# Performance work log

Measured on AMD Instinct MI355X. Metric: run time of the kernel, lower is better.

## Reference

```python
import jax, jax.numpy as jnp
import numpy as np

N, E, D, V, MAX_EDGES, G, ITERS = 50000, 200000, 128, 2000, 3, 256, 2


def _mlp3(h, W1, b1, W2, b2, W3, b3):
    h = jax.nn.relu(h @ W1 + b1)
    h = jax.nn.relu(h @ W2 + b2)
    return jax.nn.relu(h @ W3 + b3)


def _enc(ids, emb, W1, b1, W2, b2):
    h = emb[ids]
    h = jax.nn.relu(h @ W1 + b1)
    return jax.nn.relu(h @ W2 + b2)


def setup_inputs():
    key = jax.random.key(0)
    ks = iter(jax.random.split(key, 64))

    def p(shape):
        return jax.random.normal(next(ks), shape, jnp.float32) * 0.02

    inp = {
        'x': jax.random.randint(next(ks), (N,), 0, V),
        'edge_index': jax.random.randint(next(ks), (2, E), 0, N),
        'edge_attr': jax.random.randint(next(ks), (E,), 0, MAX_EDGES),
        'batch_vec': jnp.sort(jax.random.randint(next(ks), (N,), 0, G)),
        'emb_node': p((V, 2 * D)), 'Wn1': p((2 * D, D)), 'bn1': jnp.zeros((D,), jnp.float32),
        'Wn2': p((D, D)), 'bn2': jnp.zeros((D,), jnp.float32),
        'emb_edge': p((MAX_EDGES, 2 * D)), 'We1': p((2 * D, D)), 'be1': jnp.zeros((D,), jnp.float32),
        'We2': p((D, D)), 'be2': jnp.zeros((D,), jnp.float32),
    }
    for tag in ('p', 'c', 'f'):  # parent_agg, child_agg, final_agg 3-layer MLPs
        inp['W' + tag + '1'] = p((3 * D, 2 * D)); inp['b' + tag + '1'] = jnp.zeros((2 * D,), jnp.float32)
        inp['W' + tag + '2'] = p((2 * D, D)); inp['b' + tag + '2'] = jnp.zeros((D,), jnp.float32)
        inp['W' + tag + '3'] = p((D, D)); inp['b' + tag + '3'] = jnp.zeros((D,), jnp.float32)
    inp['Wo1'] = p((D, 4 * D)); inp['bo1'] = jnp.zeros((4 * D,), jnp.float32)
    inp['Wo2'] = p((4 * D, 8 * D)); inp['bo2'] = jnp.zeros((8 * D,), jnp.float32)
    return inp


def reference(x, edge_index, edge_attr, batch_vec, emb_node, Wn1, bn1, Wn2, bn2,
              emb_edge, We1, be1, We2, be2,
              Wp1, bp1, Wp2, bp2, Wp3, bp3,
              Wc1, bc1, Wc2, bc2, Wc3, bc3,
              Wf1, bf1, Wf2, bf2, Wf3, bf3,
              Wo1, bo1, Wo2, bo2):
    nodes = _enc(x, emb_node, Wn1, bn1, Wn2, bn2)       # [N, D]
    ea = _enc(edge_attr, emb_edge, We1, be1, We2, be2)  # [E, D]
    src, dst = edge_index[0], edge_index[1]
    # both aggregations normalize by degree of edge_index[0] (as in the source)
    deg = jax.ops.segment_sum(jnp.ones((E,), nodes.dtype), src, num_segments=N)
    deg_inv = jnp.where(deg > 0, 1.0 / deg, 0.0)[:, None]  # [N, 1]
    for _ in range(ITERS):
        # parent agg: flow source_to_target -> x_i = nodes[dst], x_j = nodes[src], sum at dst
        mp = _mlp3(jnp.concatenate([nodes[dst], nodes[src], ea], axis=1), Wp1, bp1, Wp2, bp2, Wp3, bp3)
        fi = deg_inv * jax.ops.segment_sum(mp, dst, num_segments=N)
        # child agg: flow target_to_source -> x_i = nodes[src], x_j = nodes[dst], sum at src
        mc = _mlp3(jnp.concatenate([nodes[src], nodes[dst], ea], axis=1), Wc1, bc1, Wc2, bc2, Wc3, bc3)
        fo = deg_inv * jax.ops.segment_sum(mc, src, num_segments=N)
        upd = _mlp3(jnp.concatenate([nodes, fi, fo], axis=1), Wf1, bf1, Wf2, bf2, Wf3, bf3)
        nodes = nodes + upd
    h = jax.nn.relu(nodes @ Wo1 + bo1)
    h = jax.nn.relu(h @ Wo2 + bo2)                      # [N, 8D]
    return jax.ops.segment_max(h, batch_vec, num_segments=G)  # global max pool [G, 8D]
```

## Files before the change

### kernel.cpp

```cpp
#include <hip/hip_runtime.h>

#define NN 50000
#define NE 200000
#define DD 128
#define GG 256
#define NITERS 2
#define NBINS 50176
#define NPART 196

typedef unsigned short u16;
typedef unsigned int u32;
typedef __bf16 bf16x8 __attribute__((ext_vector_type(8)));
typedef float f32x4 __attribute__((ext_vector_type(4)));

union U16x8 { uint4 u; bf16x8 v; u16 s[8]; };

__device__ __forceinline__ u16 f2b(float f) {
    u32 u = __float_as_uint(f);
    return (u16)((u + 0x7FFFu + ((u >> 16) & 1u)) >> 16);
}
__device__ __forceinline__ float b2f(u16 s) { return __uint_as_float(((u32)s) << 16); }

__device__ __forceinline__ uint2 pack4(const float* v) {
    uint2 r;
    r.x = (u32)f2b(v[0]) | ((u32)f2b(v[1]) << 16);
    r.y = (u32)f2b(v[2]) | ((u32)f2b(v[3]) << 16);
    return r;
}

__device__ __forceinline__ void gload_lds16(const void* g, void* lds) {
    __builtin_amdgcn_global_load_lds((const __attribute__((address_space(1))) void*)g,
                                     (__attribute__((address_space(3))) void*)lds, 16, 0, 0);
}

__device__ __forceinline__ int xcd_swz(int orig, int nwg) {
    int q = nwg >> 3, r = nwg & 7;
    int x = orig & 7, loc = orig >> 3;
    return (x < r ? x * (q + 1) : r * (q + 1) + (x - r) * q) + loc;
}

template<int K, int NL, int EPI, bool RELU, int LDN>
__global__ __launch_bounds__(256) void expand_k(
    const u16* __restrict__ A, const uint4* __restrict__ wfrag,
    const float* __restrict__ bias, float* __restrict__ of, u16* __restrict__ ob,
    int M)
{
    constexpr int KS = K / 32;
    __shared__ uint4 smem[K * 16];
    const int t = threadIdx.x, l = t & 63, wv = t >> 6;
    const int mh = wv >> 1, nh = wv & 1;
    const int mblk = blockIdx.x;
    const int c = blockIdx.y;

    #pragma unroll
    for (int i = 0; i < K / 16; ++i) {
        int s = t + 256 * i;
        int ln = s & 63, mt = (s >> 6) & 7, ksl = s >> 9;
        int row = mblk * 128 + mt * 16 + (ln & 15);
        if (row >= M) row = M - 1;
        int kk = ksl * 32 + (ln >> 4) * 8;
        gload_lds16(A + (size_t)row * K + kk, &smem[s - ln]);
    }
    __syncthreads();

    f32x4 acc[4][4] = {};
    #pragma unroll
    for (int ksl = 0; ksl < KS; ++ksl) {
        uint4 wa[4];
        #pragma unroll
        for (int mi = 0; mi < 4; ++mi)
            wa[mi] = wfrag[(size_t)((c * KS + ksl) * 8 + mh * 4 + mi) * 64 + l];
        bf16x8 bn[4];
        #pragma unroll
        for (int ni = 0; ni < 4; ++ni) { U16x8 u; u.u = smem[(ksl * 8 + nh * 4 + ni) * 64 + l]; bn[ni] = u.v; }
        #pragma unroll
        for (int mi = 0; mi < 4; ++mi) {
            U16x8 u; u.u = wa[mi];
            #pragma unroll
            for (int ni = 0; ni < 4; ++ni)
                acc[mi][ni] = __builtin_amdgcn_mfma_f32_16x16x32_bf16(u.v, bn[ni], acc[mi][ni], 0, 0, 0);
        }
    }
    float4 bb[4];
    #pragma unroll
    for (int mi = 0; mi < 4; ++mi) {
        if (bias) bb[mi] = *(const float4*)(bias + c * 128 + mh * 64 + mi * 16 + 4 * (l >> 4));
        else { bb[mi].x = 0.f; bb[mi].y = 0.f; bb[mi].z = 0.f; bb[mi].w = 0.f; }
    }
    #pragma unroll
    for (int ni = 0; ni < 4; ++ni) {
        int node = mblk * 128 + nh * 64 + ni * 16 + (l & 15);
        if (node >= M) continue;
        #pragma unroll
        for (int mi = 0; mi < 4; ++mi) {
            int col = c * 128 + mh * 64 + mi * 16 + 4 * (l >> 4);
            float v[4];
            const float* bf = &bb[mi].x;
            #pragma unroll
            for (int r = 0; r < 4; ++r) {
                v[r] = acc[mi][ni][r] + bf[r];
                if (RELU) v[r] = fmaxf(v[r], 0.f);
            }
            if (EPI == 0) {
                *(uint2*)(ob + (size_t)node * LDN + col) = pack4(v);
            } else {
                size_t a = (size_t)node * 128 + col;
                if (EPI == 2) {
                    float4 old = *(const float4*)(of + a);
                    v[0] += old.x; v[1] += old.y; v[2] += old.z; v[3] += old.w;
                }
                float4 s4; s4.x = v[0]; s4.y = v[1]; s4.z = v[2]; s4.w = v[3];
                *(float4*)(of + a) = s4;
                *(uint2*)(ob + a) = pack4(v);
            }
        }
    }
}

struct SrcBf16 {
    static constexpr bool DIRECT = true;
    const u16* A; int K;
    __device__ const void* gaddr(int row, int kk) const { return A + (size_t)row * K + kk; }
    __device__ bf16x8 operator()(int row, int kk) const {
        U16x8 u; u.u = *(const uint4*)(A + (size_t)row * K + kk); return u.v;
    }
};
struct SrcEnc {
    static constexpr bool DIRECT = false;
    const float* emb; const int* xids;
    __device__ const void* gaddr(int, int) const { return nullptr; }
    __device__ bf16x8 operator()(int row, int kk) const {
        int n = xids[row];
        const float* p = emb + (size_t)n * 256 + kk;
        float4 f0 = *(const float4*)p, f1 = *(const float4*)(p + 4);
        U16x8 r;
        r.s[0]=f2b(f0.x); r.s[1]=f2b(f0.y); r.s[2]=f2b(f0.z); r.s[3]=f2b(f0.w);
        r.s[4]=f2b(f1.x); r.s[5]=f2b(f1.y); r.s[6]=f2b(f1.z); r.s[7]=f2b(f1.w);
        return r.v;
    }
};
struct SrcUpd {
    static constexpr bool DIRECT = false;
    const float* nodes; const float* fi; const float* fo; const int* deg;
    __device__ const void* gaddr(int, int) const { return nullptr; }
    __device__ bf16x8 operator()(int row, int kk) const {
        const float* s; float sc = 1.f;
        if (kk < 128) s = nodes + (size_t)row * 128 + kk;
        else {
            int d = deg[row];
            sc = d > 0 ? 1.f / (float)d : 0.f;
            s = (kk < 256) ? fi + (size_t)row * 128 + (kk - 128)
                           : fo + (size_t)row * 128 + (kk - 256);
        }
        float4 f0 = *(const float4*)s, f1 = *(const float4*)(s + 4);
        U16x8 r;
        r.s[0]=f2b(f0.x*sc); r.s[1]=f2b(f0.y*sc); r.s[2]=f2b(f0.z*sc); r.s[3]=f2b(f0.w*sc);
        r.s[4]=f2b(f1.x*sc); r.s[5]=f2b(f1.y*sc); r.s[6]=f2b(f1.z*sc); r.s[7]=f2b(f1.w*sc);
        return r.v;
    }
};

struct EpiArgs { float* of; u16* ob; const int* idx; int ldN; };

template<int KDIM, int NBLK, int EPI, bool RELU, class SRC>
__global__ __launch_bounds__(256) void gemm_k(SRC src, const uint4* __restrict__ wfrag,
                                              const float* __restrict__ bias,
                                              EpiArgs ea, int M)
{
    constexpr int KS = KDIM / 32;
    constexpr int NPANEL = KDIM / 64;
    __shared__ uint4 smem[2048];
    const int t = threadIdx.x;
    const int l = t & 63;
    const int wv = t >> 6;
    const int mh = wv >> 1, nh = wv & 1;
    const int ell = xcd_swz(blockIdx.x, gridDim.x);
    const int mblk = ell / NBLK, nblk = ell % NBLK;

    f32x4 acc[4][4] = {};

    for (int p = 0; p < NPANEL; ++p) {
        __syncthreads();
        if constexpr (SRC::DIRECT) {
            #pragma unroll
            for (int i = 0; i < 4; ++i) {
                int s = t + 256 * i;
                int ln = s & 63, mt = (s >> 6) & 7, ksl = s >> 9;
                int row = mblk * 128 + mt * 16 + (ln & 15);
                if (row >= M) row = M - 1;
                int kk = p * 64 + ksl * 32 + (ln >> 4) * 8;
                gload_lds16(src.gaddr(row, kk), &smem[s - ln]);
            }
        } else {
            #pragma unroll
            for (int i = 0; i < 4; ++i) {
                int s = t + 256 * i;
                int ln = s & 63, mt = (s >> 6) & 7, ksl = s >> 9;
                int row = mblk * 128 + mt * 16 + (ln & 15);
                if (row >= M) row = M - 1;
                int kk = p * 64 + ksl * 32 + (ln >> 4) * 8;
                U16x8 u; u.v = src(row, kk);
                smem[s] = u.u;
            }
        }
        {
            const uint4* wp = wfrag + (size_t)(nblk * KS + 2 * p) * 512;
            #pragma unroll
            for (int i = 0; i < 4; ++i) {
                int s = t + 256 * i;
                gload_lds16(wp + s, &smem[1024 + (s - (s & 63))]);
            }
        }
        __syncthreads();
        #pragma unroll
        for (int ksl = 0; ksl < 2; ++ksl) {
            bf16x8 a[4], b[4];
            #pragma unroll
            for (int mi = 0; mi < 4; ++mi) { U16x8 u; u.u = smem[(ksl*8 + mh*4 + mi)*64 + l]; a[mi] = u.v; }
            #pragma unroll
            for (int ni = 0; ni < 4; ++ni) { U16x8 u; u.u = smem[1024 + (ksl*8 + nh*4 + ni)*64 + l]; b[ni] = u.v; }
            #pragma unroll
            for (int mi = 0; mi < 4; ++mi)
                #pragma unroll
                for (int ni = 0; ni < 4; ++ni)
                    acc[mi][ni] = __builtin_amdgcn_mfma_f32_16x16x32_bf16(a[mi], b[ni], acc[mi][ni], 0, 0, 0);
        }
    }

    float bcol[4];
    #pragma unroll
    for (int ni = 0; ni < 4; ++ni)
        bcol[ni] = bias ? bias[nblk * 128 + nh * 64 + ni * 16 + (l & 15)] : 0.f;

    if (EPI == 0) {
        __syncthreads();
        u16* bn = (u16*)smem;
        #pragma unroll
        for (int mi = 0; mi < 4; ++mi)
            #pragma unroll
            for (int ni = 0; ni < 4; ++ni)
                #pragma unroll
                for (int r = 0; r < 4; ++r) {
                    int rl = mh * 64 + mi * 16 + (l >> 4) * 4 + r;
                    int cl = nh * 64 + ni * 16 + (l & 15);
                    float v = acc[mi][ni][r] + bcol[ni];
                    if (RELU) v = fmaxf(v, 0.f);
                    int sx = (rl >> 2) & 7;
                    bn[rl * 128 + ((((cl >> 3) ^ sx)) << 3) + (cl & 7)] = f2b(v);
                }
        __syncthreads();
        int row = t >> 1, half = t & 1;
        int grow = mblk * 128 + row;
        if (grow < M) {
            int sx = (row >> 2) & 7;
            uint4* dst = (uint4*)(ea.ob + (size_t)grow * ea.ldN + nblk * 128 + half * 64);
            const uint4* sp = ((const uint4*)bn) + row * 16;
            #pragma unroll
            for (int i = 0; i < 8; ++i) dst[i] = sp[(half * 8 + i) ^ sx];
        }
    } else if (EPI == 3) {
        int g16[4][4];
        #pragma unroll
        for (int mi = 0; mi < 4; ++mi) {
            int rb = mblk * 128 + mh * 64 + mi * 16 + (l >> 4) * 4;
            #pragma unroll
            for (int r = 0; r < 4; ++r)
                g16[mi][r] = (rb + r < M) ? ea.idx[rb + r] : -1;
        }
        #pragma unroll
        for (int ni = 0; ni < 4; ++ni) {
            int colg = nblk * 128 + nh * 64 + ni * 16 + (l & 15);
            float mv = 0.f; int cg = -1;
            #pragma unroll
            for (int mi = 0; mi < 4; ++mi)
                #pragma unroll
                for (int r = 0; r < 4; ++r) {
                    float v = acc[mi][ni][r] + bcol[ni];
                    if (RELU) v = fmaxf(v, 0.f);
                    int g = g16[mi][r];
                    if (g != cg) {
                        if (cg >= 0) atomicMax((u32*)(ea.of + (size_t)cg * 1024 + colg), __float_as_uint(mv));
                        cg = g; mv = v;
                    } else mv = fmaxf(mv, v);
                }
            if (cg >= 0) atomicMax((u32*)(ea.of + (size_t)cg * 1024 + colg), __float_as_uint(mv));
        }
    }
}

__global__ __launch_bounds__(256) void edge_fused(
    const u16* __restrict__ P, const float* __restrict__ T,
    const uint4* __restrict__ W2f, const float* __restrict__ b2,
    const uint4* __restrict__ W3f, const float* __restrict__ b3,
    const int* __restrict__ idxA, const int* __restrict__ idxB,
    const int* __restrict__ eattr, float* __restrict__ agg)
{
    __shared__ uint4 smA[2048];
    __shared__ int   sidx[3][128];
    __shared__ float sT[768];
    const int t = threadIdx.x;
    const int l = t & 63;
    const int wv = t >> 6;
    const int mh = wv >> 1, nh = wv & 1;
    const int base = xcd_swz(blockIdx.x, gridDim.x) * 128;

    if (t < 128) {
        int e = (base + t < NE) ? base + t : NE - 1;
        sidx[0][t] = idxA[e];
        sidx[1][t] = idxB[e];
        sidx[2][t] = eattr[e];
    }
    for (int i = t; i < 768; i += 256) sT[i] = T[i];
    __syncthreads();

    const int rt0 = wv * 16 + (l & 15);
    const int rt1 = (wv + 4) * 16 + (l & 15);
    const int klo = (l >> 4) * 8;
    const u16* pA[2] = { P + (size_t)sidx[0][rt0] * 512, P + (size_t)sidx[0][rt1] * 512 };
    const u16* pB[2] = { P + (size_t)sidx[1][rt0] * 512 + 256, P + (size_t)sidx[1][rt1] * 512 + 256 };
    const float* pT[2] = { sT + sidx[2][rt0] * 256, sT + sidx[2][rt1] * 256 };

    uint4 ra[4], rb[4];
    #pragma unroll
    for (int i = 0; i < 4; ++i) {
        int kk = (i >> 1) * 32 + klo;
        ra[i] = *(const uint4*)(pA[i & 1] + kk);
        rb[i] = *(const uint4*)(pB[i & 1] + kk);
    }

    f32x4 acc[4][4] = {};
    #pragma unroll
    for (int p = 0; p < 4; ++p) {
        #pragma unroll
        for (int i = 0; i < 4; ++i) {
            int kk = (i >> 1) * 32 + klo;
            U16x8 ua, ub, r;
            ua.u = ra[i]; ub.u = rb[i];
            const float* tb = pT[i & 1] + p * 64 + kk;
            #pragma unroll
            for (int j = 0; j < 8; ++j) {
                float v = b2f(ua.s[j]) + b2f(ub.s[j]) + tb[j];
                r.s[j] = f2b(fmaxf(v, 0.f));
            }
            smA[(p & 1) * 1024 + t + 256 * i] = r.u;
            if (p < 3) {
                int kn = (p + 1) * 64 + kk;
                ra[i] = *(const uint4*)(pA[i & 1] + kn);
                rb[i] = *(const uint4*)(pB[i & 1] + kn);
            }
        }
        asm volatile("s_waitcnt lgkmcnt(0)" ::: "memory");
        __builtin_amdgcn_s_barrier();
        uint4 bw[2][4];
        #pragma unroll
        for (int ksl = 0; ksl < 2; ++ksl)
            #pragma unroll
            for (int ni = 0; ni < 4; ++ni)
                bw[ksl][ni] = W2f[(size_t)((p * 2 + ksl) * 8 + nh * 4 + ni) * 64 + l];
        #pragma unroll
        for (int ksl = 0; ksl < 2; ++ksl) {
            bf16x8 a[4];
            #pragma unroll
            for (int mi = 0; mi < 4; ++mi) { U16x8 u; u.u = smA[(p & 1) * 1024 + (ksl*8 + mh*4 + mi)*64 + l]; a[mi] = u.v; }
            #pragma unroll
            for (int mi = 0; mi < 4; ++mi)
                #pragma unroll
                for (int ni = 0; ni < 4; ++ni) {
                    U16x8 u; u.u = bw[ksl][ni];
                    acc[mi][ni] = __builtin_amdgcn_mfma_f32_16x16x32_bf16(a[mi], u.v, acc[mi][ni], 0, 0, 0);
                }
        }
    }

    float bc2[4];
    #pragma unroll
    for (int ni = 0; ni < 4; ++ni) bc2[ni] = b2[nh * 64 + ni * 16 + (l & 15)];
    __builtin_amdgcn_s_barrier();
    u16* bn = (u16*)smA;
    #pragma unroll
    for (int mi = 0; mi < 4; ++mi)
        #pragma unroll
        for (int ni = 0; ni < 4; ++ni)
            #pragma unroll
            for (int r = 0; r < 4; ++r) {
                int rl = mh * 64 + mi * 16 + (l >> 4) * 4 + r;
                int cl = nh * 64 + ni * 16 + (l & 15);
                float v = fmaxf(acc[mi][ni][r] + bc2[ni], 0.f);
                int sx = (rl >> 2) & 7;
                bn[rl * 128 + (((cl >> 3) ^ sx) << 3) + (cl & 7)] = f2b(v);
            }
    asm volatile("s_waitcnt lgkmcnt(0)" ::: "memory");
    __builtin_amdgcn_s_barrier();

    f32x4 acc2[4][4] = {};
    #pragma unroll
    for (int ks = 0; ks < 4; ++ks) {
        uint4 bw[4];
        #pragma unroll
        for (int ni = 0; ni < 4; ++ni)
            bw[ni] = W3f[(size_t)(ks * 8 + nh * 4 + ni) * 64 + l];
        bf16x8 a[4];
        #pragma unroll
        for (int mi = 0; mi < 4; ++mi) {
            int rl = (mh * 4 + mi) * 16 + (l & 15);
            int c0 = ks * 32 + (l >> 4) * 8;
            int sx = (rl >> 2) & 7;
            U16x8 u; u.u = *(const uint4*)&bn[rl * 128 + (((c0 >> 3) ^ sx) << 3)];
            a[mi] = u.v;
        }
        #pragma unroll
        for (int mi = 0; mi < 4; ++mi)
            #pragma unroll
            for (int ni = 0; ni < 4; ++ni) {
                U16x8 u; u.u = bw[ni];
                acc2[mi][ni] = __builtin_amdgcn_mfma_f32_16x16x32_bf16(a[mi], u.v, acc2[mi][ni], 0, 0, 0);
            }
    }

    float bc3[4];
    #pragma unroll
    for (int ni = 0; ni < 4; ++ni) bc3[ni] = b3[nh * 64 + ni * 16 + (l & 15)];
    #pragma unroll
    for (int mi = 0; mi < 4; ++mi) {
        int rt4 = mh * 64 + mi * 16 + (l >> 4) * 4;
        int nd[4];
        #pragma unroll
        for (int r = 0; r < 4; ++r)
            nd[r] = (base + rt4 + r < NE) ? sidx[0][rt4 + r] : -1;
        #pragma unroll
        for (int ni = 0; ni < 4; ++ni) {
            int col = nh * 64 + ni * 16 + (l & 15);
            float mv = 0.f; int cg = -1;
            #pragma unroll
            for (int r = 0; r < 4; ++r) {
                float v = fmaxf(acc2[mi][ni][r] + bc3[ni], 0.f);
                if (nd[r] != cg) {
                    if (cg >= 0) atomicAdd(agg + (size_t)cg * 128 + col, mv);
                    cg = nd[r]; mv = v;
                } else mv += v;
            }
            if (cg >= 0) atomicAdd(agg + (size_t)cg * 128 + col, mv);
        }
    }
}

__global__ void hist2_kernel(const int* __restrict__ dstI, const int* __restrict__ srcI,
                             int* __restrict__ hist)
{
    int i = blockIdx.x * 256 + threadIdx.x;
    if (i < NE) atomicAdd(&hist[dstI[i]], 1);
    else if (i < 2 * NE) atomicAdd(&hist[NBINS + srcI[i - NE]], 1);
}
__global__ void chunk_sum(const int* __restrict__ h, int* __restrict__ part)
{
    __shared__ int sh[256];
    int t = threadIdx.x, b = blockIdx.x;
    sh[t] = h[b * 256 + t];
    __syncthreads();
    for (int o = 128; o > 0; o >>= 1) { if (t < o) sh[t] += sh[t + o]; __syncthreads(); }
    if (t == 0) part[b] = sh[0];
}
__global__ void scan_part2(int* part)
{
    __shared__ int sh[256];
    int t = threadIdx.x, b = blockIdx.x;
    int* p = part + b * NPART;
    sh[t] = (t < NPART) ? p[t] : 0;
    __syncthreads();
    for (int o = 1; o < 256; o <<= 1) {
        int x = (t >= o) ? sh[t - o] : 0;
        __syncthreads(); sh[t] += x; __syncthreads();
    }
    if (t < NPART) p[t] = (t ? sh[t - 1] : 0) + b * NE;
}
__global__ void mk_cursor(const int* __restrict__ h, const int* __restrict__ part,
                          int* __restrict__ cur)
{
    __shared__ int sh[256];
    int t = threadIdx.x, b = blockIdx.x;
    int v = h[b * 256 + t];
    sh[t] = v;
    __syncthreads();
    for (int o = 1; o < 256; o <<= 1) {
        int x = (t >= o) ? sh[t - o] : 0;
        __syncthreads(); sh[t] += x; __syncthreads();
    }
    cur[b * 256 + t] = part[b] + sh[t] - v;
}
__global__ void sort_scatter2(const int* __restrict__ dstI, const int* __restrict__ srcI,
                              const int* __restrict__ at, int* __restrict__ cur,
                              int* __restrict__ oA, int* __restrict__ oB, int* __restrict__ oC)
{
    int i = blockIdx.x * 256 + threadIdx.x;
    if (i < NE) {
        int k = dstI[i];
        int p = atomicAdd(&cur[k], 1);
        oA[p] = k; oB[p] = srcI[i]; oC[p] = at[i];
    } else if (i < 2 * NE) {
        int e = i - NE;
        int k = srcI[e];
        int p = atomicAdd(&cur[NBINS + k], 1);
        oA[p] = k; oB[p] = dstI[e]; oC[p] = at[e];
    }
}

struct PackPtrs { const float* p[13]; };

__global__ void pack_all(PackPtrs pp, uint4* __restrict__ frag)
{
    int tid = blockIdx.x * 256 + threadIdx.x;
    if (tid >= 126976) return;
    constexpr int NJ = 15;
    const int   start[NJ] = {0,4096,6144,10240,14336,18432,22528,26624,28672,32768,34816,47104,51200,53248,61440};
    const int   fbase[NJ] = {0,4096,6144,6144,14336,14336,22528,26624,28672,32768,34816,47104,51200,53248,61440};
    const short wsel [NJ] = {0,1,2,2,3,3,4,5,6,7,8,9,10,11,12};
    const short ldt  [NJ] = {128,128,256,256,256,256,128,128,128,128,256,128,128,512,1024};
    const short rot  [NJ] = {0,0,0,128,0,128,0,0,0,0,0,0,0,0,0};
    const short cot  [NJ] = {0,0,0,-256,0,-256,0,0,0,0,0,0,0,0,0};
    const short nbst [NJ] = {0,0,0,2,0,2,0,0,0,0,0,0,0,0,0};
    const short kst  [NJ] = {8,4,4,4,4,4,8,4,8,4,12,8,4,4,16};
    int j = 0;
    for (int i = NJ - 1; i >= 1; --i) if (tid >= start[i]) { j = i; break; }
    int rem = tid - start[j];
    int KS = kst[j];
    int nbrel = rem / (KS * 512);
    int r1 = rem % (KS * 512);
    int ks = r1 >> 9;
    int r2 = r1 & 511;
    int nt = r2 >> 6, l = r2 & 63;
    int nb = nbst[j] + nbrel;
    int k  = ks * 32 + (l >> 4) * 8;
    int ld = ldt[j];
    int col = nb * 128 + nt * 16 + (l & 15) + cot[j];
    const float* W = pp.p[wsel[j]];
    U16x8 u;
    #pragma unroll
    for (int jj = 0; jj < 8; ++jj) u.s[jj] = f2b(W[(size_t)(rot[j] + k + jj) * ld + col]);
    frag[fbase[j] + ((size_t)(nb * KS + ks) * 8 + nt) * 64 + l] = u.u;
}

__global__ void enc_tab_kernel(const float* __restrict__ emb_edge,
                               const float* __restrict__ We1, const float* __restrict__ be1,
                               const float* __restrict__ We2, const float* __restrict__ be2,
                               const float* __restrict__ Wp1, const float* __restrict__ bp1,
                               const float* __restrict__ Wc1, const float* __restrict__ bc1,
                               float* __restrict__ Tp, float* __restrict__ Tc)
{
    __shared__ float h1[3][128];
    __shared__ float ea[3][128];
    const int t = threadIdx.x;
    if (t < 128) {
        for (int a = 0; a < 3; ++a) {
            float s = be1[t];
            for (int k = 0; k < 256; ++k) s = fmaf(emb_edge[a * 256 + k], We1[k * 128 + t], s);
            h1[a][t] = fmaxf(s, 0.f);
        }
    }
    __syncthreads();
    if (t < 128) {
        for (int a = 0; a < 3; ++a) {
            float s = be2[t];
            for (int k = 0; k < 128; ++k) s = fmaf(h1[a][k], We2[k * 128 + t], s);
            ea[a][t] = fmaxf(s, 0.f);
        }
    }
    __syncthreads();
    for (int a = 0; a < 3; ++a) {
        float sp = bp1[t], sc = bc1[t];
        for (int k = 0; k < 128; ++k) {
            float e = ea[a][k];
            sp = fmaf(e, Wp1[(size_t)(256 + k) * 256 + t], sp);
            sc = fmaf(e, Wc1[(size_t)(256 + k) * 256 + t], sc);
        }
        Tp[a * 256 + t] = sp;
        Tc[a * 256 + t] = sc;
    }
}

extern "C" void kernel_launch(void* const* d_in, const int* in_sizes, int n_in,
                              void* d_out, int out_size, void* d_ws, size_t ws_size,
                              hipStream_t stream)
{
    const int*   x          = (const int*)d_in[0];
    const int*   edge_index = (const int*)d_in[1];
    const int*   edge_attr  = (const int*)d_in[2];
    const int*   batch_vec  = (const int*)d_in[3];
    const float* emb_node   = (const float*)d_in[4];
    const float* Wn1 = (const float*)d_in[5];  const float* bn1 = (const float*)d_in[6];
    const float* Wn2 = (const float*)d_in[7];  const float* bn2 = (const float*)d_in[8];
    const float* emb_edge = (const float*)d_in[9];
    const float* We1 = (const float*)d_in[10]; const float* be1 = (const float*)d_in[11];
    const float* We2 = (const float*)d_in[12]; const float* be2 = (const float*)d_in[13];
    const float* Wp1 = (const float*)d_in[14]; const float* bp1 = (const float*)d_in[15];
    const float* Wp2 = (const float*)d_in[16]; const float* bp2 = (const float*)d_in[17];
    const float* Wp3 = (const float*)d_in[18]; const float* bp3 = (const float*)d_in[19];
    const float* Wc1 = (const float*)d_in[20]; const float* bc1 = (const float*)d_in[21];
    const float* Wc2 = (const float*)d_in[22]; const float* bc2 = (const float*)d_in[23];
    const float* Wc3 = (const float*)d_in[24]; const float* bc3 = (const float*)d_in[25];
    const float* Wf1 = (const float*)d_in[26]; const float* bf1 = (const float*)d_in[27];
    const float* Wf2 = (const float*)d_in[28]; const float* bf2 = (const float*)d_in[29];
    const float* Wf3 = (const float*)d_in[30]; const float* bf3 = (const float*)d_in[31];
    const float* Wo1 = (const float*)d_in[32]; const float* bo1 = (const float*)d_in[33];
    const float* Wo2 = (const float*)d_in[34]; const float* bo2 = (const float*)d_in[35];

    float* out = (float*)d_out;

    char* w = (char*)d_ws;
    auto alloc = [&](size_t bytes) { char* p = w; w += (bytes + 255) & ~(size_t)255; return p; };
    float* nodes   = (float*)alloc((size_t)NN * DD * 4);
    u16*   nodesbf = (u16*)  alloc((size_t)NN * DD * 2);
    float* fi      = (float*)alloc((size_t)NN * DD * 4);
    float* fo      = (float*)alloc((size_t)NN * DD * 4);
    u16*   P       = (u16*)  alloc((size_t)NN * 512 * 2);
    u16*   h2      = (u16*)  alloc((size_t)NN * 384 * 2);
    float* Tp      = (float*)alloc(3 * 256 * 4);
    float* Tc      = (float*)alloc(3 * 256 * 4);
    uint4* frag    = (uint4*)alloc((size_t)126976 * 16);
    int* hist = (int*)alloc((size_t)2 * NBINS * 4);
    int* part = (int*)alloc((size_t)2 * NPART * 4);
    int* cur  = (int*)alloc((size_t)2 * NBINS * 4);
    int* sA   = (int*)alloc((size_t)2 * NE * 4);
    int* sB   = (int*)alloc((size_t)2 * NE * 4);
    int* sC   = (int*)alloc((size_t)2 * NE * 4);

    u16* He = h2;
    u16* U1 = h2;
    u16* U2 = h2 + (size_t)NN * 256;
    u16* Hout1 = P;
    const int* degS = hist + NBINS;

    uint4* Wn1f = frag;
    uint4* Wn2f = Wn1f + 4096;
    uint4* PWp  = Wn2f + 2048;
    uint4* PWc  = PWp  + 8192;
    uint4* W2p  = PWc  + 8192;
    uint4* W3p  = W2p  + 4096;
    uint4* W2c  = W3p  + 2048;
    uint4* W3c  = W2c  + 4096;
    uint4* Wf1f = W3c  + 2048;
    uint4* Wf2f = Wf1f + 12288;
    uint4* Wf3f = Wf2f + 4096;
    uint4* Wo1f = Wf3f + 2048;
    uint4* Wo2f = Wo1f + 8192;

    const int* srcI = edge_index;
    const int* dstI = edge_index + NE;

    const int MB50 = (NN + 127) / 128;
    const int MBE  = (NE + 127) / 128;

    (void)hipMemsetAsync(d_out, 0, (size_t)out_size * 4, stream);
    (void)hipMemsetAsync(hist, 0, (size_t)2 * NBINS * 4, stream);

    PackPtrs pp;
    pp.p[0]=Wn1; pp.p[1]=Wn2; pp.p[2]=Wp1; pp.p[3]=Wc1; pp.p[4]=Wp2; pp.p[5]=Wp3;
    pp.p[6]=Wc2; pp.p[7]=Wc3; pp.p[8]=Wf1; pp.p[9]=Wf2; pp.p[10]=Wf3; pp.p[11]=Wo1; pp.p[12]=Wo2;
    pack_all<<<(126976 + 255) / 256, 256, 0, stream>>>(pp, frag);

    enc_tab_kernel<<<1, 256, 0, stream>>>(emb_edge, We1, be1, We2, be2,
                                          Wp1, bp1, Wc1, bc1, Tp, Tc);

    hist2_kernel<<<(2 * NE + 255) / 256, 256, 0, stream>>>(dstI, srcI, hist);
    chunk_sum<<<2 * NPART, 256, 0, stream>>>(hist, part);
    scan_part2<<<2, 256, 0, stream>>>(part);
    mk_cursor<<<2 * NPART, 256, 0, stream>>>(hist, part, cur);
    sort_scatter2<<<(2 * NE + 255) / 256, 256, 0, stream>>>(dstI, srcI, edge_attr, cur, sA, sB, sC);

    gemm_k<256, 1, 0, true, SrcEnc><<<MB50, 256, 0, stream>>>(
        SrcEnc{emb_node, x}, Wn1f, bn1, EpiArgs{nullptr, He, nullptr, 128}, NN);
    expand_k<128, 1, 1, true, 128><<<dim3(MB50, 1), 256, 0, stream>>>(
        He, Wn2f, bn2, nodes, nodesbf, NN);

    for (int it = 0; it < NITERS; ++it) {
        (void)hipMemsetAsync(fi, 0, (size_t)2 * NN * DD * 4, stream);

        expand_k<128, 4, 0, false, 512><<<dim3(MB50, 4), 256, 0, stream>>>(
            nodesbf, PWp, nullptr, nullptr, P, NN);
        edge_fused<<<MBE, 256, 0, stream>>>(P, Tp, W2p, bp2, W3p, bp3,
                                            sA, sB, sC, fi);

        expand_k<128, 4, 0, false, 512><<<dim3(MB50, 4), 256, 0, stream>>>(
            nodesbf, PWc, nullptr, nullptr, P, NN);
        edge_fused<<<MBE, 256, 0, stream>>>(P, Tc, W2c, bc2, W3c, bc3,
                                            sA + NE, sB + NE, sC + NE, fo);

        gemm_k<384, 2, 0, true, SrcUpd><<<MB50 * 2, 256, 0, stream>>>(
            SrcUpd{nodes, fi, fo, degS}, Wf1f, bf1, EpiArgs{nullptr, U1, nullptr, 256}, NN);
        expand_k<256, 1, 0, true, 128><<<dim3(MB50, 1), 256, 0, stream>>>(
            U1, Wf2f, bf2, nullptr, U2, NN);
        expand_k<128, 1, 2, true, 128><<<dim3(MB50, 1), 256, 0, stream>>>(
            U2, Wf3f, bf3, nodes, nodesbf, NN);
    }

    expand_k<128, 4, 0, true, 512><<<dim3(MB50, 4), 256, 0, stream>>>(
        nodesbf, Wo1f, bo1, nullptr, Hout1, NN);
    gemm_k<512, 8, 3, true, SrcBf16><<<MB50 * 8, 256, 0, stream>>>(
        SrcBf16{Hout1, 512}, Wo2f, bo2, EpiArgs{out, nullptr, batch_vec, 1024}, NN);
}
```

Measured before the change: 917.0 us.

## Fold fi/fo zeroing into expand kernel and add dedicated output-head max-pool kernel

Removes the per-iteration memset of the fi/fo aggregation buffers and instead zeroes them inside the preceding expand_k launch, where each block clears its own rows and column slice. Replaces the final Wo2 GEMM (gemm_k with EPI 3, eight N-blocks per M-block each reloading the A panel) with a new outhead2_k kernel. That kernel loads a 64-row, 512-wide A tile into LDS once, loops over all eight 128-column chunks, and reads weight fragments straight from global memory before doing the segment-max atomics. This saves launches and repeated A-tile loads. In exchange it uses a larger LDS footprint per block, serial column chunks within a block, and fewer blocks in flight.

```diff
diff --git a/kernel.cpp b/kernel.cpp
--- a/kernel.cpp
+++ b/kernel.cpp
@@ -43,7 +43,7 @@
 __global__ __launch_bounds__(256) void expand_k(
     const u16* __restrict__ A, const uint4* __restrict__ wfrag,
     const float* __restrict__ bias, float* __restrict__ of, u16* __restrict__ ob,
-    int M)
+    float* __restrict__ zf, int M)
 {
     constexpr int KS = K / 32;
     __shared__ uint4 smem[K * 16];
@@ -60,6 +60,18 @@
         if (row >= M) row = M - 1;
         int kk = ksl * 32 + (ln >> 4) * 8;
         gload_lds16(A + (size_t)row * K + kk, &smem[s - ln]);
+    }
+    if (zf) {
+        #pragma unroll
+        for (int i = 0; i < 4; ++i) {
+            int f = t + 256 * i;
+            int row = f >> 3, c4 = f & 7;
+            int grow = mblk * 128 + row;
+            if (grow < M) {
+                float4 z; z.x = 0.f; z.y = 0.f; z.z = 0.f; z.w = 0.f;
+                *(float4*)(zf + (size_t)grow * 128 + c * 32 + c4 * 4) = z;
+            }
+        }
     }
     __syncthreads();
 
@@ -117,14 +129,70 @@
     }
 }
 
-struct SrcBf16 {
-    static constexpr bool DIRECT = true;
-    const u16* A; int K;
-    __device__ const void* gaddr(int row, int kk) const { return A + (size_t)row * K + kk; }
-    __device__ bf16x8 operator()(int row, int kk) const {
-        U16x8 u; u.u = *(const uint4*)(A + (size_t)row * K + kk); return u.v;
-    }
-};
+__global__ __launch_bounds__(256) void outhead2_k(
+    const u16* __restrict__ A, const uint4* __restrict__ wfrag,
+    const float* __restrict__ bias, const int* __restrict__ bvec,
+    float* __restrict__ gout, int M)
+{
+    __shared__ uint4 smem[4096];
+    __shared__ int sb[64];
+    const int t = threadIdx.x, l = t & 63, wv = t >> 6;
+    const int mh = wv >> 1, nh = wv & 1;
+    const int mblk = blockIdx.x;
+
+    if (t < 64) {
+        int r = mblk * 64 + t;
+        sb[t] = (r < M) ? bvec[r] : -1;
+    }
+    #pragma unroll
+    for (int i = 0; i < 16; ++i) {
+        int s = t + 256 * i;
+        int ln = s & 63, mt = (s >> 6) & 3, ksl = s >> 8;
+        int row = mblk * 64 + mt * 16 + (ln & 15);
+        if (row >= M) row = M - 1;
+        int kk = ksl * 32 + (ln >> 4) * 8;
+        gload_lds16(A + (size_t)row * 512 + kk, &smem[s - ln]);
+    }
+    __syncthreads();
+
+    #pragma unroll 1
+    for (int c = 0; c < 8; ++c) {
+        f32x4 acc[2][4] = {};
+        #pragma unroll
+        for (int ks = 0; ks < 16; ++ks) {
+            bf16x8 a[2];
+            #pragma unroll
+            for (int mi = 0; mi < 2; ++mi) { U16x8 u; u.u = smem[(ks * 4 + mh * 2 + mi) * 64 + l]; a[mi] = u.v; }
+            #pragma unroll
+            for (int ni = 0; ni < 4; ++ni) {
+                U16x8 u; u.u = wfrag[(size_t)((c * 16 + ks) * 8 + nh * 4 + ni) * 64 + l];
+                #pragma unroll
+                for (int mi = 0; mi < 2; ++mi)
+                    acc[mi][ni] = __builtin_amdgcn_mfma_f32_16x16x32_bf16(a[mi], u.v, acc[mi][ni], 0, 0, 0);
+            }
+        }
+        #pragma unroll
+        for (int ni = 0; ni < 4; ++ni) {
+            int colg = c * 128 + nh * 64 + ni * 16 + (l & 15);
+            float bc = bias[colg];
+            float mv = 0.f; int cg = -1;
+            #pragma unroll
+            for (int mi = 0; mi < 2; ++mi)
+                #pragma unroll
+                for (int r = 0; r < 4; ++r) {
+                    int lr = mh * 32 + mi * 16 + 4 * (l >> 4) + r;
+                    int g = sb[lr];
+                    float v = fmaxf(acc[mi][ni][r] + bc, 0.f);
+                    if (g != cg) {
+                        if (cg >= 0) atomicMax((u32*)(gout + (size_t)cg * 1024 + colg), __float_as_uint(mv));
+                        cg = g; mv = v;
+                    } else mv = fmaxf(mv, v);
+                }
+            if (cg >= 0) atomicMax((u32*)(gout + (size_t)cg * 1024 + colg), __float_as_uint(mv));
+        }
+    }
+}
+
 struct SrcEnc {
     static constexpr bool DIRECT = false;
     const float* emb; const int* xids;
@@ -181,27 +249,15 @@
 
     for (int p = 0; p < NPANEL; ++p) {
         __syncthreads();
-        if constexpr (SRC::DIRECT) {
-            #pragma unroll
-            for (int i = 0; i < 4; ++i) {
-                int s = t + 256 * i;
-                int ln = s & 63, mt = (s >> 6) & 7, ksl = s >> 9;
-                int row = mblk * 128 + mt * 16 + (ln & 15);
-                if (row >= M) row = M - 1;
-                int kk = p * 64 + ksl * 32 + (ln >> 4) * 8;
-                gload_lds16(src.gaddr(row, kk), &smem[s - ln]);
-            }
-        } else {
-            #pragma unroll
-            for (int i = 0; i < 4; ++i) {
-                int s = t + 256 * i;
-                int ln = s & 63, mt = (s >> 6) & 7, ksl = s >> 9;
-                int row = mblk * 128 + mt * 16 + (ln & 15);
-                if (row >= M) row = M - 1;
-                int kk = p * 64 + ksl * 32 + (ln >> 4) * 8;
-                U16x8 u; u.v = src(row, kk);
-                smem[s] = u.u;
-            }
+        #pragma unroll
+        for (int i = 0; i < 4; ++i) {
+            int s = t + 256 * i;
+            int ln = s & 63, mt = (s >> 6) & 7, ksl = s >> 9;
+            int row = mblk * 128 + mt * 16 + (ln & 15);
+            if (row >= M) row = M - 1;
+            int kk = p * 64 + ksl * 32 + (ln >> 4) * 8;
+            U16x8 u; u.v = src(row, kk);
+            smem[s] = u.u;
         }
         {
             const uint4* wp = wfrag + (size_t)(nblk * KS + 2 * p) * 512;
@@ -232,59 +288,30 @@
     for (int ni = 0; ni < 4; ++ni)
         bcol[ni] = bias ? bias[nblk * 128 + nh * 64 + ni * 16 + (l & 15)] : 0.f;
 
-    if (EPI == 0) {
-        __syncthreads();
-        u16* bn = (u16*)smem;
-        #pragma unroll
-        for (int mi = 0; mi < 4; ++mi)
-            #pragma unroll
-            for (int ni = 0; ni < 4; ++ni)
-                #pragma unroll
-                for (int r = 0; r < 4; ++r) {
-                    int rl = mh * 64 + mi * 16 + (l >> 4) * 4 + r;
-                    int cl = nh * 64 + ni * 16 + (l & 15);
-                    float v = acc[mi][ni][r] + bcol[ni];
-                    if (RELU) v = fmaxf(v, 0.f);
-                    int sx = (rl >> 2) & 7;
-                    bn[rl * 128 + ((((cl >> 3) ^ sx)) << 3) + (cl & 7)] = f2b(v);
-                }
-        __syncthreads();
-        int row = t >> 1, half = t & 1;
-        int grow = mblk * 128 + row;
-        if (grow < M) {
-            int sx = (row >> 2) & 7;
-            uint4* dst = (uint4*)(ea.ob + (size_t)grow * ea.ldN + nblk * 128 + half * 64);
-            const uint4* sp = ((const uint4*)bn) + row * 16;
-            #pragma unroll
-            for (int i = 0; i < 8; ++i) dst[i] = sp[(half * 8 + i) ^ sx];
-        }
-    } else if (EPI == 3) {
-        int g16[4][4];
-        #pragma unroll
-        for (int mi = 0; mi < 4; ++mi) {
-            int rb = mblk * 128 + mh * 64 + mi * 16 + (l >> 4) * 4;
-            #pragma unroll
-            for (int r = 0; r < 4; ++r)
-                g16[mi][r] = (rb + r < M) ? ea.idx[rb + r] : -1;
-        }
-        #pragma unroll
-        for (int ni = 0; ni < 4; ++ni) {
-            int colg = nblk * 128 + nh * 64 + ni * 16 + (l & 15);
-            float mv = 0.f; int cg = -1;
-            #pragma unroll
-            for (int mi = 0; mi < 4; ++mi)
-                #pragma unroll
-                for (int r = 0; r < 4; ++r) {
-                    float v = acc[mi][ni][r] + bcol[ni];
-                    if (RELU) v = fmaxf(v, 0.f);
-                    int g = g16[mi][r];
-                    if (g != cg) {
-                        if (cg >= 0) atomicMax((u32*)(ea.of + (size_t)cg * 1024 + colg), __float_as_uint(mv));
-                        cg = g; mv = v;
-                    } else mv = fmaxf(mv, v);
-                }
-            if (cg >= 0) atomicMax((u32*)(ea.of + (size_t)cg * 1024 + colg), __float_as_uint(mv));
-        }
+    __syncthreads();
+    u16* bn = (u16*)smem;
+    #pragma unroll
+    for (int mi = 0; mi < 4; ++mi)
+        #pragma unroll
+        for (int ni = 0; ni < 4; ++ni)
+            #pragma unroll
+            for (int r = 0; r < 4; ++r) {
+                int rl = mh * 64 + mi * 16 + (l >> 4) * 4 + r;
+                int cl = nh * 64 + ni * 16 + (l & 15);
+                float v = acc[mi][ni][r] + bcol[ni];
+                if (RELU) v = fmaxf(v, 0.f);
+                int sx = (rl >> 2) & 7;
+                bn[rl * 128 + ((((cl >> 3) ^ sx)) << 3) + (cl & 7)] = f2b(v);
+            }
+    __syncthreads();
+    int row = t >> 1, half = t & 1;
+    int grow = mblk * 128 + row;
+    if (grow < M) {
+        int sx = (row >> 2) & 7;
+        uint4* dst = (uint4*)(ea.ob + (size_t)grow * ea.ldN + nblk * 128 + half * 64);
+        const uint4* sp = ((const uint4*)bn) + row * 16;
+        #pragma unroll
+        for (int i = 0; i < 8; ++i) dst[i] = sp[(half * 8 + i) ^ sx];
     }
 }
 
@@ -648,6 +675,7 @@
 
     const int MB50 = (NN + 127) / 128;
     const int MBE  = (NE + 127) / 128;
+    const int MB64 = (NN + 63) / 64;
 
     (void)hipMemsetAsync(d_out, 0, (size_t)out_size * 4, stream);
     (void)hipMemsetAsync(hist, 0, (size_t)2 * NBINS * 4, stream);
@@ -669,31 +697,28 @@
     gemm_k<256, 1, 0, true, SrcEnc><<<MB50, 256, 0, stream>>>(
         SrcEnc{emb_node, x}, Wn1f, bn1, EpiArgs{nullptr, He, nullptr, 128}, NN);
     expand_k<128, 1, 1, true, 128><<<dim3(MB50, 1), 256, 0, stream>>>(
-        He, Wn2f, bn2, nodes, nodesbf, NN);
+        He, Wn2f, bn2, nodes, nodesbf, nullptr, NN);
 
     for (int it = 0; it < NITERS; ++it) {
-        (void)hipMemsetAsync(fi, 0, (size_t)2 * NN * DD * 4, stream);
-
         expand_k<128, 4, 0, false, 512><<<dim3(MB50, 4), 256, 0, stream>>>(
-            nodesbf, PWp, nullptr, nullptr, P, NN);
+            nodesbf, PWp, nullptr, nullptr, P, fi, NN);
         edge_fused<<<MBE, 256, 0, stream>>>(P, Tp, W2p, bp2, W3p, bp3,
                                             sA, sB, sC, fi);
 
         expand_k<128, 4, 0, false, 512><<<dim3(MB50, 4), 256, 0, stream>>>(
-            nodesbf, PWc, nullptr, nullptr, P, NN);
+            nodesbf, PWc, nullptr, nullptr, P, fo, NN);
         edge_fused<<<MBE, 256, 0, stream>>>(P, Tc, W2c, bc2, W3c, bc3,
                                             sA + NE, sB + NE, sC + NE, fo);
 
         gemm_k<384, 2, 0, true, SrcUpd><<<MB50 * 2, 256, 0, stream>>>(
             SrcUpd{nodes, fi, fo, degS}, Wf1f, bf1, EpiArgs{nullptr, U1, nullptr, 256}, NN);
         expand_k<256, 1, 0, true, 128><<<dim3(MB50, 1), 256, 0, stream>>>(
-            U1, Wf2f, bf2, nullptr, U2, NN);
+            U1, Wf2f, bf2, nullptr, U2, nullptr, NN);
         expand_k<128, 1, 2, true, 128><<<dim3(MB50, 1), 256, 0, stream>>>(
-            U2, Wf3f, bf3, nodes, nodesbf, NN);
+            U2, Wf3f, bf3, nodes, nodesbf, nullptr, NN);
     }
 
     expand_k<128, 4, 0, true, 512><<<dim3(MB50, 4), 256, 0, stream>>>(
-        nodesbf, Wo1f, bo1, nullptr, Hout1, NN);
-    gemm_k<512, 8, 3, true, SrcBf16><<<MB50 * 8, 256, 0, stream>>>(
-        SrcBf16{Hout1, 512}, Wo2f, bo2, EpiArgs{out, nullptr, batch_vec, 1024}, NN);
-}
+        nodesbf, Wo1f, bo1, nullptr, Hout1, nullptr, NN);
+    outhead2_k<<<MB64, 256, 0, stream>>>(Hout1, Wo2f, bo2, batch_vec, out, NN);
+}
```

Result: slower. 982.0 us (+7.1%).
